# Performance work log

Hardware: AMD Instinct MI355X
Metric: run time of the kernel (lower is better)

The kernel has to match this reference:

```python
import jax, jax.numpy as jnp
import numpy as np

B = 8192  # number of covariance matrices
N = 64    # n_assets


def setup_inputs() -> dict:
    key = jax.random.key(0)
    A = jax.random.normal(key, (B, N, N), dtype=jnp.float32)
    # SPD covariance: A A^T / N + 0.1 I  (real covariances are SPD)
    sigma = jnp.einsum('bij,bkj->bik', A, A) / N + 0.1 * jnp.eye(N, dtype=jnp.float32)
    return {"sigma": sigma}


def reference(sigma) -> jnp.ndarray:
    # Symmetrize, as the original does: 0.5 * (S + S^T)
    sym = 0.5 * (sigma + jnp.swapaxes(sigma, -1, -2))  # [B, N, N]
    n = sym.shape[-1]
    ones = jnp.ones((*sym.shape[:-2], n), dtype=sym.dtype)  # [B, N]
    # Closed-form min-variance (short selling allowed): w = S^-1 1 / (1^T S^-1 1)
    z = jnp.linalg.solve(sym, ones[..., None])[..., 0]      # [B, N]
    w = z / jnp.sum(z, axis=-1, keepdims=True)              # [B, N]
    return w[..., None]  # [B, N, 1], matching expand_dims(axis=-1)
```

## Files before the change

kernel.cpp:

```cpp
#include <hip/hip_runtime.h>


#define NN 64

typedef float v2f __attribute__((ext_vector_type(2)));
typedef float v4f __attribute__((ext_vector_type(4)));

template <int I> struct ic { static constexpr int value = I; };

template <int Start, int End, typename F>
__device__ __forceinline__ void static_for(F&& f) {
    if constexpr (Start < End) {
        f(ic<Start>{});
        static_for<Start + 1, End>(static_cast<F&&>(f));
    }
}

__device__ __forceinline__ float rlane(float v, int lane) {
    return __int_as_float(__builtin_amdgcn_readlane(__float_as_int(v), lane));
}

__device__ __forceinline__ float frcp(float x) {
#if __has_builtin(__builtin_amdgcn_rcpf)
    return __builtin_amdgcn_rcpf(x);
#else
    return 1.0f / x;
#endif
}

__device__ __forceinline__ v2f fma2(v2f a, v2f b, v2f c) {
#if __has_builtin(__builtin_elementwise_fma)
    return __builtin_elementwise_fma(a, b, c);
#else
    v2f r; r.x = fmaf(a.x, b.x, c.x); r.y = fmaf(a.y, b.y, c.y); return r;
#endif
}

__global__ __launch_bounds__(256) void minvar_kernel(const float* __restrict__ sigma,
                                                     float* __restrict__ out,
                                                     int batch) {
    __shared__ float pb[4][2][2 * NN * 4 / 2];

    const int lane = threadIdx.x & 63;
    const int wid  = threadIdx.x >> 6;
    const int bid  = blockIdx.x * 4 + wid;
    if (bid >= batch) return;

    const float* __restrict__ p = sigma + (size_t)bid * (NN * NN) + (size_t)lane * NN;

    v2f r[NN / 2];
    static_for<0, NN / 4>([&](auto j4c) {
        constexpr int j4 = decltype(j4c)::value;
        v4f v = reinterpret_cast<const v4f*>(p)[j4];
        r[2 * j4 + 0] = v2f{v.x, v.y};
        r[2 * j4 + 1] = v2f{v.z, v.w};
    });

    float b = 1.0f;
    const int wbase = (lane >> 1) * 8 + (lane & 1);

    static_for<0, 16>([&](auto pc) {
        constexpr int P  = decltype(pc)::value;
        constexpr int k0 = 4 * P;
        constexpr int m0 = 2 * P;
        float* __restrict__ wb = &pb[wid][P & 1][0];

        const float el0  = r[m0].x;
        const float piv0 = rlane(el0, k0);
        const float nf0  = (lane > k0) ? (-el0 * frcp(piv0)) : 0.0f;
        b = fmaf(nf0, rlane(b, k0), b);
        const float u01 = rlane(r[m0].y,     k0);
        const float u02 = rlane(r[m0 + 1].x, k0);
        const float u03 = rlane(r[m0 + 1].y, k0);
        r[m0].y     = fmaf(nf0, u01, r[m0].y);
        r[m0 + 1].x = fmaf(nf0, u02, r[m0 + 1].x);
        r[m0 + 1].y = fmaf(nf0, u03, r[m0 + 1].y);

        const float el1  = r[m0].y;
        const float piv1 = rlane(el1, k0 + 1);
        const float nf1  = (lane > k0 + 1) ? (-el1 * frcp(piv1)) : 0.0f;
        b = fmaf(nf1, rlane(b, k0 + 1), b);
        const float u12 = rlane(r[m0 + 1].x, k0 + 1);
        const float u13 = rlane(r[m0 + 1].y, k0 + 1);
        r[m0 + 1].x = fmaf(nf1, u12, r[m0 + 1].x);
        r[m0 + 1].y = fmaf(nf1, u13, r[m0 + 1].y);

        const float el2  = r[m0 + 1].x;
        const float piv2 = rlane(el2, k0 + 2);
        const float nf2  = (lane > k0 + 2) ? (-el2 * frcp(piv2)) : 0.0f;
        b = fmaf(nf2, rlane(b, k0 + 2), b);
        const float u23 = rlane(r[m0 + 1].y, k0 + 2);
        r[m0 + 1].y = fmaf(nf2, u23, r[m0 + 1].y);

        const float el3  = r[m0 + 1].y;
        const float piv3 = rlane(el3, k0 + 3);
        const float nf3  = (lane > k0 + 3) ? (-el3 * frcp(piv3)) : 0.0f;
        b = fmaf(nf3, rlane(b, k0 + 3), b);

        if constexpr (P < 15) {
            wb[wbase + 0] = el0;
            wb[wbase + 2] = el1;
            wb[wbase + 4] = el2;
            wb[wbase + 6] = el3;

            const v2f n0 = v2f{nf0, nf0}, n1 = v2f{nf1, nf1};
            const v2f n2 = v2f{nf2, nf2}, n3 = v2f{nf3, nf3};
            static_for<m0 + 2, NN / 2>([&](auto mc) {
                constexpr int m = decltype(mc)::value;
                const v4f lo = *reinterpret_cast<const v4f*>(wb + 8 * m);
                const v4f hi = *reinterpret_cast<const v4f*>(wb + 8 * m + 4);
                v2f acc = r[m];
                acc = fma2(n0, v2f{lo.x, lo.y}, acc);
                acc = fma2(n1, v2f{lo.z, lo.w}, acc);
                acc = fma2(n2, v2f{hi.x, hi.y}, acc);
                acc = fma2(n3, v2f{hi.z, hi.w}, acc);
                r[m] = acc;
            });
        }
    });

    static_for<0, NN>([&](auto kk) {
        constexpr int k  = NN - 1 - decltype(kk)::value;
        constexpr int pk = k / 2;
        const float ekk = (k & 1) ? r[pk].y : r[pk].x;
        const float ukk = rlane(ekk, k);
        const float yk  = rlane(b, k);
        const float zk  = yk * frcp(ukk);
        const float upd = (lane < k) ? (-ekk) : 0.0f;
        b = (lane == k) ? zk : fmaf(upd, zk, b);
    });

    float tot = b;
    #pragma unroll
    for (int off = 32; off >= 1; off >>= 1)
        tot += __shfl_xor(tot, off, 64);

    out[(size_t)bid * NN + lane] = b * frcp(tot);
}

extern "C" void kernel_launch(void* const* d_in, const int* in_sizes, int n_in,
                              void* d_out, int out_size, void* d_ws, size_t ws_size,
                              hipStream_t stream) {
    const float* sigma = (const float*)d_in[0];
    float* out = (float*)d_out;
    const int batch  = in_sizes[0] / (NN * NN);
    const int blocks = (batch + 3) / 4;
    minvar_kernel<<<blocks, 256, 0, stream>>>(sigma, out, batch);
}
```

Before: 201.4 us.

## Replace Gaussian elimination plus back-substitution with Gauss-Jordan diagonal solve

The elimination now applies each pivot's update to every row except the pivot row, not just the rows below it. This reduces the matrix to diagonal form, so the solution becomes a single per-lane division by the saved pivot. It removes the 64-step serial back-substitution loop, with its readlanes and dependent updates, while the trailing-update FMA count per lane stays the same. The shared-memory stores of pivot-column elements are also moved earlier so they can overlap with the pivot computation.

```diff
diff --git a/kernel.cpp b/kernel.cpp
--- a/kernel.cpp
+++ b/kernel.cpp
@@ -57,6 +57,7 @@
     });
 
     float b = 1.0f;
+    float d = 1.0f;
     const int wbase = (lane >> 1) * 8 + (lane & 1);
 
     static_for<0, 16>([&](auto pc) {
@@ -66,8 +67,10 @@
         float* __restrict__ wb = &pb[wid][P & 1][0];
 
         const float el0  = r[m0].x;
+        if constexpr (P < 15) wb[wbase + 0] = el0;
         const float piv0 = rlane(el0, k0);
-        const float nf0  = (lane > k0) ? (-el0 * frcp(piv0)) : 0.0f;
+        const float nf0  = (lane != k0) ? (-el0 * frcp(piv0)) : 0.0f;
+        d = (lane == k0) ? el0 : d;
         b = fmaf(nf0, rlane(b, k0), b);
         const float u01 = rlane(r[m0].y,     k0);
         const float u02 = rlane(r[m0 + 1].x, k0);
@@ -77,8 +80,10 @@
         r[m0 + 1].y = fmaf(nf0, u03, r[m0 + 1].y);
 
         const float el1  = r[m0].y;
+        if constexpr (P < 15) wb[wbase + 2] = el1;
         const float piv1 = rlane(el1, k0 + 1);
-        const float nf1  = (lane > k0 + 1) ? (-el1 * frcp(piv1)) : 0.0f;
+        const float nf1  = (lane != k0 + 1) ? (-el1 * frcp(piv1)) : 0.0f;
+        d = (lane == k0 + 1) ? el1 : d;
         b = fmaf(nf1, rlane(b, k0 + 1), b);
         const float u12 = rlane(r[m0 + 1].x, k0 + 1);
         const float u13 = rlane(r[m0 + 1].y, k0 + 1);
@@ -86,23 +91,22 @@
         r[m0 + 1].y = fmaf(nf1, u13, r[m0 + 1].y);
 
         const float el2  = r[m0 + 1].x;
+        if constexpr (P < 15) wb[wbase + 4] = el2;
         const float piv2 = rlane(el2, k0 + 2);
-        const float nf2  = (lane > k0 + 2) ? (-el2 * frcp(piv2)) : 0.0f;
+        const float nf2  = (lane != k0 + 2) ? (-el2 * frcp(piv2)) : 0.0f;
+        d = (lane == k0 + 2) ? el2 : d;
         b = fmaf(nf2, rlane(b, k0 + 2), b);
         const float u23 = rlane(r[m0 + 1].y, k0 + 2);
         r[m0 + 1].y = fmaf(nf2, u23, r[m0 + 1].y);
 
         const float el3  = r[m0 + 1].y;
+        if constexpr (P < 15) wb[wbase + 6] = el3;
         const float piv3 = rlane(el3, k0 + 3);
-        const float nf3  = (lane > k0 + 3) ? (-el3 * frcp(piv3)) : 0.0f;
+        const float nf3  = (lane != k0 + 3) ? (-el3 * frcp(piv3)) : 0.0f;
+        d = (lane == k0 + 3) ? el3 : d;
         b = fmaf(nf3, rlane(b, k0 + 3), b);
 
         if constexpr (P < 15) {
-            wb[wbase + 0] = el0;
-            wb[wbase + 2] = el1;
-            wb[wbase + 4] = el2;
-            wb[wbase + 6] = el3;
-
             const v2f n0 = v2f{nf0, nf0}, n1 = v2f{nf1, nf1};
             const v2f n2 = v2f{nf2, nf2}, n3 = v2f{nf3, nf3};
             static_for<m0 + 2, NN / 2>([&](auto mc) {
@@ -119,23 +123,14 @@
         }
     });
 
-    static_for<0, NN>([&](auto kk) {
-        constexpr int k  = NN - 1 - decltype(kk)::value;
-        constexpr int pk = k / 2;
-        const float ekk = (k & 1) ? r[pk].y : r[pk].x;
-        const float ukk = rlane(ekk, k);
-        const float yk  = rlane(b, k);
-        const float zk  = yk * frcp(ukk);
-        const float upd = (lane < k) ? (-ekk) : 0.0f;
-        b = (lane == k) ? zk : fmaf(upd, zk, b);
-    });
+    const float z = b * frcp(d);
 
-    float tot = b;
+    float tot = z;
     #pragma unroll
     for (int off = 32; off >= 1; off >>= 1)
         tot += __shfl_xor(tot, off, 64);
 
-    out[(size_t)bid * NN + lane] = b * frcp(tot);
+    out[(size_t)bid * NN + lane] = z * frcp(tot);
 }
 
 extern "C" void kernel_launch(void* const* d_in, const int* in_sizes, int n_in,
```

After: 217.9 us. 8.2% more time.
